# Performance work log

Measured on AMD Instinct MI355X. Metric: run time of the kernel, lower is better.

Reference implementation:

```python
import jax, jax.numpy as jnp
import numpy as np

NUM_HEADS = 8
GROUPS = 8
EPS = 1e-5


def setup_inputs() -> dict:
    key = jax.random.key(0)
    ks = jax.random.split(key, 5)
    B, C, H, W = 2, 512, 64, 64
    x = jax.random.normal(ks[0], (B, C, H, W), dtype=jnp.float32)
    gn_w = jnp.ones((C,), dtype=jnp.float32)
    gn_b = jnp.zeros((C,), dtype=jnp.float32)
    qkv_w = jax.random.normal(ks[1], (3 * C, C), dtype=jnp.float32) * 0.02  # 1x1 conv weight
    qkv_b = jnp.zeros((3 * C,), dtype=jnp.float32)
    proj_w = jax.random.normal(ks[2], (C, C), dtype=jnp.float32) * 0.02
    proj_b = jnp.zeros((C,), dtype=jnp.float32)
    return {"x": x, "gn_w": gn_w, "gn_b": gn_b, "qkv_w": qkv_w,
            "qkv_b": qkv_b, "proj_w": proj_w, "proj_b": proj_b}


def group_norm(x, w, b):
    B, C, H, W = x.shape
    xg = x.reshape(B, GROUPS, C // GROUPS, H, W)
    mean = xg.mean(axis=(2, 3, 4), keepdims=True)
    var = xg.var(axis=(2, 3, 4), keepdims=True)  # biased, matching torch GroupNorm
    h = ((xg - mean) * jax.lax.rsqrt(var + EPS)).reshape(B, C, H, W)
    return h * w[None, :, None, None] + b[None, :, None, None]


def reference(x, gn_w, gn_b, qkv_w, qkv_b, proj_w, proj_b):
    B, C, H, W = x.shape
    nh = NUM_HEADS
    dh = C // nh
    scale = dh ** -0.5
    S = H * W

    h = group_norm(x, gn_w, gn_b)
    # 1x1 conv == per-pixel linear: (B,3C,H,W)
    qkv = jnp.einsum('bchw,oc->bohw', h, qkv_w) + qkv_b[None, :, None, None]
    qkv = qkv.reshape(B, 3, nh, dh, S)
    q = jnp.swapaxes(qkv[:, 0], -1, -2)  # (B, nh, S, dh)
    k = jnp.swapaxes(qkv[:, 1], -1, -2)
    v = jnp.swapaxes(qkv[:, 2], -1, -2)

    attn = jax.nn.softmax(jnp.einsum('bhsd,btd->bhst', q, k.reshape(B * nh, S, dh).reshape(B, nh, S, dh)) * scale, axis=-1) if False else jax.nn.softmax(jnp.einsum('bhsd,bhtd->bhst', q, k) * scale, axis=-1)
    out = jnp.einsum('bhst,bhtd->bhsd', attn, v)  # (B, nh, S, dh)
    out = jnp.swapaxes(out, -1, -2).reshape(B, C, H, W)
    out = jnp.einsum('bchw,oc->bohw', out, proj_w) + proj_b[None, :, None, None]
    return x + out
```

## Files before the change

kernel.cpp:

```cpp
#include <hip/hip_runtime.h>
#include <hip/hip_bf16.h>

typedef __attribute__((ext_vector_type(4)))  float  f32x4;
typedef __attribute__((ext_vector_type(16))) float  f32x16;
typedef __attribute__((ext_vector_type(8)))  short  s16x8;
typedef __attribute__((ext_vector_type(4)))  short  s16x4;
typedef __attribute__((ext_vector_type(4)))  unsigned u32x4;
typedef __attribute__((ext_vector_type(2)))  unsigned u32x2;

__device__ __forceinline__ float bf2f(short v) {
    unsigned u = ((unsigned)(unsigned short)v) << 16;
    return __builtin_bit_cast(float, u);
}
__device__ __forceinline__ short f2bf(float f) {
    unsigned u = __builtin_bit_cast(unsigned, f);
    u += 0x7fff + ((u >> 16) & 1);
    return (short)(u >> 16);
}
__device__ __forceinline__ unsigned cvt_pk_bf16(float lo, float hi) {
    unsigned r;
    asm("v_cvt_pk_bf16_f32 %0, %1, %2" : "=v"(r) : "v"(lo), "v"(hi));
    return r;
}
__device__ __forceinline__ float exp2_asm(float x) {
    float r; asm("v_exp_f32 %0, %1" : "=v"(r) : "v"(x)); return r;
}
__device__ __forceinline__ float log2_asm(float x) {
    float r; asm("v_log_f32 %0, %1" : "=v"(r) : "v"(x)); return r;
}
__device__ __forceinline__ void perm32swap(unsigned &a, unsigned &b) {
    u32x2 r = __builtin_amdgcn_permlane32_swap(a, b, false, false);
    a = r[0]; b = r[1];
}
__device__ __forceinline__ void gload16(const short* g, short* l) {
    __builtin_amdgcn_global_load_lds(
        (const __attribute__((address_space(1))) void*)g,
        (__attribute__((address_space(3))) void*)l, 16, 0, 0);
}

#define BATCH 2
#define CCH   512
#define SSP   4096
#define NH    8
#define DH    64

__global__ __launch_bounds__(256) void gn_partial_wcast_kernel(
    const float* __restrict__ x, float* __restrict__ part,
    const float* __restrict__ qw, const float* __restrict__ pw,
    short* __restrict__ dq, short* __restrict__ dp)
{
    if (blockIdx.x >= 512) {
        int idx = ((blockIdx.x - 512) * 256 + threadIdx.x) * 8;
        const float* src; short* dst;
        if (idx < 786432) { src = qw + idx; dst = dq + idx; }
        else              { src = pw + (idx - 786432); dst = dp + (idx - 786432); }
        f32x4 a = *(const f32x4*)src;
        f32x4 b = *(const f32x4*)(src + 4);
        s16x8 o;
        o[0]=f2bf(a[0]); o[1]=f2bf(a[1]); o[2]=f2bf(a[2]); o[3]=f2bf(a[3]);
        o[4]=f2bf(b[0]); o[5]=f2bf(b[1]); o[6]=f2bf(b[2]); o[7]=f2bf(b[3]);
        *(s16x8*)dst = o;
        return;
    }
    int bg = blockIdx.x >> 5, chunk = blockIdx.x & 31;
    const float* base = x + (size_t)bg * 262144 + chunk * 8192;
    int t = threadIdx.x, lane = t & 63, wave = t >> 6;
    float s = 0.f, ss = 0.f;
    #pragma unroll
    for (int k = 0; k < 8; ++k) {
        f32x4 v = *(const f32x4*)&base[k * 1024 + t * 4];
        #pragma unroll
        for (int j = 0; j < 4; ++j) { s += v[j]; ss += v[j] * v[j]; }
    }
    #pragma unroll
    for (int mask = 1; mask < 64; mask <<= 1) {
        s  += __shfl_xor(s,  mask);
        ss += __shfl_xor(ss, mask);
    }
    __shared__ float rs[4], rss[4];
    if (lane == 0) { rs[wave] = s; rss[wave] = ss; }
    __syncthreads();
    if (t == 0) {
        part[blockIdx.x * 2]     = rs[0] + rs[1] + rs[2] + rs[3];
        part[blockIdx.x * 2 + 1] = rss[0] + rss[1] + rss[2] + rss[3];
    }
}

__global__ void gn_final_kernel(const float* __restrict__ part, float* __restrict__ stats)
{
    int t = threadIdx.x;
    if (t < 16) {
        float s = 0.f, ss = 0.f;
        for (int c = 0; c < 32; ++c) {
            s  += part[(t * 32 + c) * 2];
            ss += part[(t * 32 + c) * 2 + 1];
        }
        float mean = s * (1.f / 262144.f);
        float var  = ss * (1.f / 262144.f) - mean * mean;
        stats[t * 2]     = mean;
        stats[t * 2 + 1] = rsqrtf(var + 1e-5f);
    }
}

__global__ __launch_bounds__(256) void gn_apply_kernel(
    const float* __restrict__ x, const float* __restrict__ gw, const float* __restrict__ gb,
    const float* __restrict__ stats, short* __restrict__ hbuf)
{
    __shared__ float tile[64][65];
    int id = blockIdx.x;
    int st = id & 63, ct = (id >> 6) & 7, b = id >> 9;
    int t  = threadIdx.x;
    float mean = stats[(b * 8 + ct) * 2], rstd = stats[(b * 8 + ct) * 2 + 1];
    #pragma unroll
    for (int pass = 0; pass < 4; ++pass) {
        int cr = pass * 16 + (t >> 4);
        int c  = ct * 64 + cr;
        f32x4 v = *(const f32x4*)&x[((size_t)(b * CCH + c)) * SSP + st * 64 + (t & 15) * 4];
        float w  = gw[c] * rstd;
        float bb = gb[c] - mean * w;
        #pragma unroll
        for (int j = 0; j < 4; ++j) tile[cr][(t & 15) * 4 + j] = v[j] * w + bb;
    }
    __syncthreads();
    int sr = t >> 2, cc0 = (t & 3) * 16;
    s16x8 o0, o1;
    #pragma unroll
    for (int j = 0; j < 8; ++j) {
        o0[j] = f2bf(tile[cc0 + j][sr]);
        o1[j] = f2bf(tile[cc0 + 8 + j][sr]);
    }
    short* dst = &hbuf[(size_t)(b * SSP + st * 64 + sr) * CCH + ct * 64 + cc0];
    *(s16x8*)dst = o0;
    *(s16x8*)(dst + 8) = o1;
}

template<int EPI>
__global__ __launch_bounds__(256) void gemm_bt_kernel(
    const short* __restrict__ A, const short* __restrict__ Bt,
    const float* __restrict__ bias,
    short* __restrict__ qout, short* __restrict__ kout, short* __restrict__ vout,
    const float* __restrict__ xres, float* __restrict__ out,
    int K)
{
    __shared__ short As[4096], Bs[4096];
    const int t = threadIdx.x;
    const int lane = t & 63, wave = t >> 6;
    const int wm = wave >> 1, wn = wave & 1;
    const int m0 = blockIdx.x * 128, n0 = blockIdx.y * 128;
    const int l15 = lane & 15, lq = lane >> 4;

    f32x4 acc[4][4];
    #pragma unroll
    for (int i = 0; i < 4; ++i)
        #pragma unroll
        for (int j = 0; j < 4; ++j) acc[i][j] = (f32x4){0.f, 0.f, 0.f, 0.f};

    for (int kk = 0; kk < K; kk += 32) {
        __syncthreads();
        #pragma unroll
        for (int i = 0; i < 2; ++i) {
            int idx = i * 256 + t;
            int row = idx >> 2, cb = idx & 3;
            int dst = ((row >> 4) << 9) + ((((row & 15)) | (cb << 4)) << 3);
            *(s16x8*)&As[dst] = *(const s16x8*)&A [(size_t)(m0 + row) * K + kk + cb * 8];
            *(s16x8*)&Bs[dst] = *(const s16x8*)&Bt[(size_t)(n0 + row) * K + kk + cb * 8];
        }
        __syncthreads();
        s16x8 af[4], bfr[4];
        #pragma unroll
        for (int mt = 0; mt < 4; ++mt) af[mt]  = *(const s16x8*)&As[(((wm * 4 + mt) << 9) + lane * 8)];
        #pragma unroll
        for (int nt = 0; nt < 4; ++nt) bfr[nt] = *(const s16x8*)&Bs[(((wn * 4 + nt) << 9) + lane * 8)];
        #pragma unroll
        for (int mt = 0; mt < 4; ++mt)
            #pragma unroll
            for (int nt = 0; nt < 4; ++nt)
                acc[mt][nt] = __builtin_amdgcn_mfma_f32_16x16x32_bf16(af[mt], bfr[nt], acc[mt][nt], 0, 0, 0);
    }

    #pragma unroll
    for (int mt = 0; mt < 4; ++mt) {
        const int r0 = m0 + wm * 64 + mt * 16 + lq * 4;
        #pragma unroll
        for (int nt = 0; nt < 4; ++nt) {
            const int c = n0 + wn * 64 + nt * 16 + l15;
            float bv = bias[c];
            if (EPI == 0) {
                int bb = r0 >> 12, tloc = r0 & 4095;
                if (c < 512) {
                    #pragma unroll
                    for (int i = 0; i < 4; ++i)
                        qout[(size_t)(r0 + i) * 512 + c] = f2bf(acc[mt][nt][i] + bv);
                } else if (c < 1024) {
                    int hh = (c - 512) >> 6, d = (c - 512) & 63;
                    int T = tloc >> 6, tb = (tloc >> 5) & 1;
                    size_t base = (((size_t)(bb * 8 + hh) * 64 + T) * 8 + tb * 4 + (d >> 4)) * 512
                                  + 256 * ((d >> 3) & 1) + (d & 7);
                    #pragma unroll
                    for (int i = 0; i < 4; ++i)
                        kout[base + ((tloc & 31) + i) * 8] = f2bf(acc[mt][nt][i] + bv);
                } else {
                    int hh = (c - 1024) >> 6, d = (c - 1024) & 63;
                    int T = tloc >> 6, s = (tloc >> 4) & 3, thi = (tloc >> 3) & 1, j0 = tloc & 7;
                    size_t base = (((size_t)(bb * 8 + hh) * 64 + T) * 8 + (d >> 5) * 4 + s) * 512
                                  + ((d & 31) + 32 * thi) * 8 + j0;
                    s16x4 pv;
                    #pragma unroll
                    for (int i = 0; i < 4; ++i) pv[i] = f2bf(acc[mt][nt][i] + bv);
                    *(s16x4*)&vout[base] = pv;
                }
            } else {
                int bb = r0 >> 12, s = r0 & 4095;
                size_t xi = (size_t)(bb * CCH + c) * SSP + s;
                f32x4 xv = *(const f32x4*)&xres[xi];
                f32x4 o  = xv + acc[mt][nt] + bv;
                *(f32x4*)&out[xi] = o;
            }
        }
    }
}

__global__ __launch_bounds__(256, 4) void attn_kernel(
    const short* __restrict__ qbuf, const short* __restrict__ kfrag,
    const short* __restrict__ vfrag,
    short* __restrict__ p0, short* __restrict__ p1, float* __restrict__ aout)
{
    __shared__ short Ks[2][4096];
    __shared__ short Vs[2][4096];
    const int t = threadIdx.x, lane = t & 63, wave = t >> 6;
    const int flat = blockIdx.y * 32 + blockIdx.x;
    const int p = flat >> 3;
    const int yy = (flat & 7) * 4 + (p & 3);
    const int qblk = p >> 2;
    const int bh = yy & 15, half = yy >> 4;
    const int b = bh >> 3, h = bh & 7;
    const int q0w = qblk * 128 + wave * 32;
    const int l31 = lane & 31, lh = lane >> 5;
    const int kv0 = half * 2048;

    s16x8 qf[4];
    {
        const short* qp = qbuf + (size_t)(b * SSP + q0w + l31) * 512 + h * 64 + 8 * lh;
        #pragma unroll
        for (int s = 0; s < 4; ++s) {
            s16x8 raw = *(const s16x8*)(qp + 16 * s);
            #pragma unroll
            for (int j = 0; j < 8; ++j) qf[s][j] = f2bf(bf2f(raw[j]) * 0.18033688011112042f);
        }
    }

    const short* kbase = kfrag + (size_t)bh * 262144 + lane * 8;
    const short* vbase = vfrag + (size_t)bh * 262144 + lane * 8;

    f32x16 oacc[2];
    oacc[0] = (f32x16){}; oacc[1] = (f32x16){};
    f32x16 lacc = (f32x16){};

    s16x8 ones;
    #pragma unroll
    for (int j = 0; j < 8; ++j) ones[j] = (short)0x3F80;

    {
        const short* kg = kbase + (size_t)(kv0 >> 6) * 4096 + wave * 1024;
        gload16(kg,       &Ks[0][wave * 1024]);
        gload16(kg + 512, &Ks[0][wave * 1024 + 512]);
        const short* vg = vbase + (size_t)(kv0 >> 6) * 4096 + wave * 1024;
        gload16(vg,       &Vs[0][wave * 1024]);
        gload16(vg + 512, &Vs[0][wave * 1024 + 512]);
    }
    asm volatile("s_waitcnt vmcnt(0)" ::: "memory");
    __syncthreads();

    int cur = 0;
    for (int t0 = kv0; t0 < kv0 + 2048; t0 += 64) {
        if (t0 + 64 < kv0 + 2048) {
            int nb = cur ^ 1;
            const short* kg = kbase + (size_t)((t0 + 64) >> 6) * 4096 + wave * 1024;
            gload16(kg,       &Ks[nb][wave * 1024]);
            gload16(kg + 512, &Ks[nb][wave * 1024 + 512]);
            const short* vg = vbase + (size_t)((t0 + 64) >> 6) * 4096 + wave * 1024;
            gload16(vg,       &Vs[nb][wave * 1024]);
            gload16(vg + 512, &Vs[nb][wave * 1024 + 512]);
        }

        f32x16 sacc0 = (f32x16){}, sacc1 = (f32x16){};
        __builtin_amdgcn_s_setprio(1);
        #pragma unroll
        for (int s = 0; s < 4; ++s) {
            s16x8 k0 = *(const s16x8*)&Ks[cur][(0 + s) * 512 + lane * 8];
            s16x8 k1 = *(const s16x8*)&Ks[cur][(4 + s) * 512 + lane * 8];
            sacc0 = __builtin_amdgcn_mfma_f32_32x32x16_bf16(k0, qf[s], sacc0, 0, 0, 0);
            sacc1 = __builtin_amdgcn_mfma_f32_32x32x16_bf16(k1, qf[s], sacc1, 0, 0, 0);
        }
        __builtin_amdgcn_s_setprio(0);

        #pragma unroll
        for (int r = 0; r < 16; ++r) { sacc0[r] = exp2_asm(sacc0[r]); sacc1[r] = exp2_asm(sacc1[r]); }

        unsigned w[16];
        #pragma unroll
        for (int r = 0; r < 8; ++r) {
            w[r]     = cvt_pk_bf16(sacc0[2 * r], sacc0[2 * r + 1]);
            w[8 + r] = cvt_pk_bf16(sacc1[2 * r], sacc1[2 * r + 1]);
        }
        #pragma unroll
        for (int s = 0; s < 4; ++s) {
            perm32swap(w[s * 4 + 0], w[s * 4 + 2]);
            perm32swap(w[s * 4 + 1], w[s * 4 + 3]);
        }

        __builtin_amdgcn_s_setprio(1);
        #pragma unroll
        for (int s = 0; s < 4; ++s) {
            u32x4 pb = { w[s * 4 + 0], w[s * 4 + 1], w[s * 4 + 2], w[s * 4 + 3] };
            s16x8 pB = __builtin_bit_cast(s16x8, pb);
            s16x8 v0v = *(const s16x8*)&Vs[cur][(0 + s) * 512 + lane * 8];
            s16x8 v1v = *(const s16x8*)&Vs[cur][(4 + s) * 512 + lane * 8];
            oacc[0] = __builtin_amdgcn_mfma_f32_32x32x16_bf16(v0v, pB, oacc[0], 0, 0, 0);
            oacc[1] = __builtin_amdgcn_mfma_f32_32x32x16_bf16(v1v, pB, oacc[1], 0, 0, 0);
            lacc    = __builtin_amdgcn_mfma_f32_32x32x16_bf16(ones, pB, lacc, 0, 0, 0);
        }
        __builtin_amdgcn_s_setprio(0);

        asm volatile("s_waitcnt vmcnt(0)" ::: "memory");
        __syncthreads();
        cur ^= 1;
    }

    short* pO = half ? p1 : p0;
    float l_ = lacc[0];
    float linv = 1.f / l_;
    int q = q0w + l31;
    size_t obase = ((size_t)bh * 4096 + q) * 64;
    #pragma unroll
    for (int db = 0; db < 2; ++db)
        #pragma unroll
        for (int g = 0; g < 4; ++g) {
            s16x4 o;
            #pragma unroll
            for (int i = 0; i < 4; ++i) o[i] = f2bf(oacc[db][g * 4 + i] * linv);
            *(s16x4*)&pO[obase + db * 32 + g * 8 + lh * 4] = o;
        }
    if (lh == 0)
        aout[half * 65536 + bh * 4096 + q] = log2_asm(l_);
}

__global__ __launch_bounds__(256) void combine_kernel(
    const short* __restrict__ p0, const short* __restrict__ p1,
    const float* __restrict__ aout, short* __restrict__ ao)
{
    int bh = blockIdx.x >> 7, q = (blockIdx.x & 127) * 32 + (threadIdx.x >> 3);
    int d0 = (threadIdx.x & 7) * 8;
    size_t pi = ((size_t)bh * 4096 + q) * 64 + d0;
    s16x8 o1 = *(const s16x8*)&p0[pi];
    s16x8 o2 = *(const s16x8*)&p1[pi];
    float a1 = aout[bh * 4096 + q], a2 = aout[65536 + bh * 4096 + q];
    float M = fmaxf(a1, a2);
    float w1 = exp2_asm(a1 - M), w2 = exp2_asm(a2 - M);
    float inv = 1.f / (w1 + w2);
    w1 *= inv; w2 *= inv;
    s16x8 o;
    #pragma unroll
    for (int j = 0; j < 8; ++j) o[j] = f2bf(bf2f(o1[j]) * w1 + bf2f(o2[j]) * w2);
    int b = bh >> 3, h = bh & 7;
    *(s16x8*)&ao[(size_t)(b * SSP + q) * 512 + h * 64 + d0] = o;
}

extern "C" void kernel_launch(void* const* d_in, const int* in_sizes, int n_in,
                              void* d_out, int out_size, void* d_ws, size_t ws_size,
                              hipStream_t stream)
{
    (void)in_sizes; (void)n_in; (void)out_size; (void)ws_size;
    const float* x      = (const float*)d_in[0];
    const float* gn_w   = (const float*)d_in[1];
    const float* gn_b   = (const float*)d_in[2];
    const float* qkv_w  = (const float*)d_in[3];
    const float* qkv_b  = (const float*)d_in[4];
    const float* proj_w = (const float*)d_in[5];
    const float* proj_b = (const float*)d_in[6];
    float* out = (float*)d_out;
    char* ws = (char*)d_ws;

    short* hbuf  = (short*)(ws + 0);
    short* qbuf  = (short*)(ws + 8388608);
    short* kfrag = (short*)(ws + 16777216);
    short* vfrag = (short*)(ws + 25165824);
    short* aobuf = (short*)(ws + 33554432);
    short* wqkv  = (short*)(ws + 41943040);
    short* wproj = (short*)(ws + 43515904);
    float* part  = (float*)(ws + 44040192);
    float* stats = (float*)(ws + 44044288);
    float* ascal = (float*)(ws + 41943040);

    gn_partial_wcast_kernel<<<1024, 256, 0, stream>>>(x, part, qkv_w, proj_w, wqkv, wproj);
    gn_final_kernel<<<1, 64, 0, stream>>>(part, stats);
    gn_apply_kernel<<<1024, 256, 0, stream>>>(x, gn_w, gn_b, stats, hbuf);
    gemm_bt_kernel<0><<<dim3(64, 12), 256, 0, stream>>>(hbuf, wqkv, qkv_b,
                                                        qbuf, kfrag, vfrag, nullptr, nullptr, 512);
    attn_kernel<<<dim3(32, 32), 256, 0, stream>>>(qbuf, kfrag, vfrag,
                                                  hbuf, aobuf, ascal);
    combine_kernel<<<2048, 256, 0, stream>>>(hbuf, aobuf, ascal, kfrag);
    gemm_bt_kernel<1><<<dim3(64, 4), 256, 0, stream>>>(kfrag, wproj, proj_b,
                                                       nullptr, nullptr, nullptr, x, out, 512);
}
```

Measured before the change: 149.7 us.

## Fuse split-KV combine into projection GEMM A-load and double K-step

Removes the separate combine kernel. The projection GEMM now loads both partial attention outputs and their log-sum scales, merges them while staging its A tile, and writes the result straight into shared memory. This saves one launch and one write and read of the combined activation. The GEMM K-step is also raised from 32 to 64, which doubles shared memory per block and halves the number of barriers. In exchange, the combine work is recomputed by each of the 4 N-blocks that load the same A rows, and the ascal loads are per-row scattered reads.

After: 156.1 us. 1.04x slower.

```diff
diff --git a/kernel.cpp b/kernel.cpp
--- a/kernel.cpp
+++ b/kernel.cpp
@@ -136,13 +136,14 @@
 
 template<int EPI>
 __global__ __launch_bounds__(256) void gemm_bt_kernel(
-    const short* __restrict__ A, const short* __restrict__ Bt,
-    const float* __restrict__ bias,
+    const short* __restrict__ A, const short* __restrict__ Ap1,
+    const float* __restrict__ ascal,
+    const short* __restrict__ Bt, const float* __restrict__ bias,
     short* __restrict__ qout, short* __restrict__ kout, short* __restrict__ vout,
     const float* __restrict__ xres, float* __restrict__ out,
     int K)
 {
-    __shared__ short As[4096], Bs[4096];
+    __shared__ short As[8192], Bs[8192];
     const int t = threadIdx.x;
     const int lane = t & 63, wave = t >> 6;
     const int wm = wave >> 1, wn = wave & 1;
@@ -155,27 +156,51 @@
         #pragma unroll
         for (int j = 0; j < 4; ++j) acc[i][j] = (f32x4){0.f, 0.f, 0.f, 0.f};
 
-    for (int kk = 0; kk < K; kk += 32) {
+    for (int kk = 0; kk < K; kk += 64) {
         __syncthreads();
         #pragma unroll
-        for (int i = 0; i < 2; ++i) {
-            int idx = i * 256 + t;
-            int row = idx >> 2, cb = idx & 3;
-            int dst = ((row >> 4) << 9) + ((((row & 15)) | (cb << 4)) << 3);
-            *(s16x8*)&As[dst] = *(const s16x8*)&A [(size_t)(m0 + row) * K + kk + cb * 8];
+        for (int i = 0; i < 4; ++i) {
+            int slot = i * 256 + t;
+            int row = slot >> 3, cb = slot & 7;
+            int dst = ((cb >> 2) << 12) + ((row >> 4) << 9) + (((row & 15) | ((cb & 3) << 4)) << 3);
             *(s16x8*)&Bs[dst] = *(const s16x8*)&Bt[(size_t)(n0 + row) * K + kk + cb * 8];
+            if (EPI == 0) {
+                *(s16x8*)&As[dst] = *(const s16x8*)&A[(size_t)(m0 + row) * K + kk + cb * 8];
+            } else {
+                int r = m0 + row;
+                int b = r >> 12, s = r & 4095;
+                int k0 = kk + cb * 8;
+                int h = k0 >> 6, d0 = k0 & 63;
+                int qi = (b * 8 + h) * 4096 + s;
+                float a1 = ascal[qi], a2 = ascal[65536 + qi];
+                float M = fmaxf(a1, a2);
+                float w1 = exp2_asm(a1 - M), w2 = exp2_asm(a2 - M);
+                float inv = 1.f / (w1 + w2);
+                w1 *= inv; w2 *= inv;
+                size_t pi = (size_t)qi * 64 + d0;
+                s16x8 o0 = *(const s16x8*)&A[pi];
+                s16x8 o1 = *(const s16x8*)&Ap1[pi];
+                s16x8 cmb;
+                #pragma unroll
+                for (int j = 0; j < 8; ++j)
+                    cmb[j] = f2bf(bf2f(o0[j]) * w1 + bf2f(o1[j]) * w2);
+                *(s16x8*)&As[dst] = cmb;
+            }
         }
         __syncthreads();
-        s16x8 af[4], bfr[4];
-        #pragma unroll
-        for (int mt = 0; mt < 4; ++mt) af[mt]  = *(const s16x8*)&As[(((wm * 4 + mt) << 9) + lane * 8)];
-        #pragma unroll
-        for (int nt = 0; nt < 4; ++nt) bfr[nt] = *(const s16x8*)&Bs[(((wn * 4 + nt) << 9) + lane * 8)];
-        #pragma unroll
-        for (int mt = 0; mt < 4; ++mt)
+        #pragma unroll
+        for (int sub = 0; sub < 2; ++sub) {
+            s16x8 af[4], bfr[4];
             #pragma unroll
-            for (int nt = 0; nt < 4; ++nt)
-                acc[mt][nt] = __builtin_amdgcn_mfma_f32_16x16x32_bf16(af[mt], bfr[nt], acc[mt][nt], 0, 0, 0);
+            for (int mt = 0; mt < 4; ++mt) af[mt]  = *(const s16x8*)&As[(sub << 12) + ((wm * 4 + mt) << 9) + lane * 8];
+            #pragma unroll
+            for (int nt = 0; nt < 4; ++nt) bfr[nt] = *(const s16x8*)&Bs[(sub << 12) + ((wn * 4 + nt) << 9) + lane * 8];
+            #pragma unroll
+            for (int mt = 0; mt < 4; ++mt)
+                #pragma unroll
+                for (int nt = 0; nt < 4; ++nt)
+                    acc[mt][nt] = __builtin_amdgcn_mfma_f32_16x16x32_bf16(af[mt], bfr[nt], acc[mt][nt], 0, 0, 0);
+        }
     }
 
     #pragma unroll
@@ -345,27 +370,6 @@
         aout[half * 65536 + bh * 4096 + q] = log2_asm(l_);
 }
 
-__global__ __launch_bounds__(256) void combine_kernel(
-    const short* __restrict__ p0, const short* __restrict__ p1,
-    const float* __restrict__ aout, short* __restrict__ ao)
-{
-    int bh = blockIdx.x >> 7, q = (blockIdx.x & 127) * 32 + (threadIdx.x >> 3);
-    int d0 = (threadIdx.x & 7) * 8;
-    size_t pi = ((size_t)bh * 4096 + q) * 64 + d0;
-    s16x8 o1 = *(const s16x8*)&p0[pi];
-    s16x8 o2 = *(const s16x8*)&p1[pi];
-    float a1 = aout[bh * 4096 + q], a2 = aout[65536 + bh * 4096 + q];
-    float M = fmaxf(a1, a2);
-    float w1 = exp2_asm(a1 - M), w2 = exp2_asm(a2 - M);
-    float inv = 1.f / (w1 + w2);
-    w1 *= inv; w2 *= inv;
-    s16x8 o;
-    #pragma unroll
-    for (int j = 0; j < 8; ++j) o[j] = f2bf(bf2f(o1[j]) * w1 + bf2f(o2[j]) * w2);
-    int b = bh >> 3, h = bh & 7;
-    *(s16x8*)&ao[(size_t)(b * SSP + q) * 512 + h * 64 + d0] = o;
-}
-
 extern "C" void kernel_launch(void* const* d_in, const int* in_sizes, int n_in,
                               void* d_out, int out_size, void* d_ws, size_t ws_size,
                               hipStream_t stream)
@@ -395,11 +399,10 @@
     gn_partial_wcast_kernel<<<1024, 256, 0, stream>>>(x, part, qkv_w, proj_w, wqkv, wproj);
     gn_final_kernel<<<1, 64, 0, stream>>>(part, stats);
     gn_apply_kernel<<<1024, 256, 0, stream>>>(x, gn_w, gn_b, stats, hbuf);
-    gemm_bt_kernel<0><<<dim3(64, 12), 256, 0, stream>>>(hbuf, wqkv, qkv_b,
+    gemm_bt_kernel<0><<<dim3(64, 12), 256, 0, stream>>>(hbuf, nullptr, nullptr, wqkv, qkv_b,
                                                         qbuf, kfrag, vfrag, nullptr, nullptr, 512);
     attn_kernel<<<dim3(32, 32), 256, 0, stream>>>(qbuf, kfrag, vfrag,
                                                   hbuf, aobuf, ascal);
-    combine_kernel<<<2048, 256, 0, stream>>>(hbuf, aobuf, ascal, kfrag);
-    gemm_bt_kernel<1><<<dim3(64, 4), 256, 0, stream>>>(kfrag, wproj, proj_b,
+    gemm_bt_kernel<1><<<dim3(64, 4), 256, 0, stream>>>(hbuf, aobuf, ascal, wproj, proj_b,
                                                        nullptr, nullptr, nullptr, x, out, 512);
 }
```
